# Performance work log

Hardware: AMD Instinct MI355X
Metric: run time of the kernel (lower is better)

## Reference

```python
import jax, jax.numpy as jnp
import numpy as np

BITS = 4
GROUP_SIZE = 128
INFEATURES = 4096
OUTFEATURES = 11008
ELEMS_PER_INT = 32 // BITS  # 8


def setup_inputs() -> dict:
    key = jax.random.key(0)
    k1, k2, k3, k4, k5 = jax.random.split(key, 5)
    x = jax.random.normal(k1, (4, 2048, INFEATURES), dtype=jnp.float32)
    # packed uint32 weights stored as int32 bit-pattern (full 32-bit random)
    qweight = jax.random.randint(k2, (OUTFEATURES, INFEATURES * BITS // 32), 0, 2147483647, dtype=jnp.int32)
    scales = jax.random.uniform(k3, (OUTFEATURES, INFEATURES // GROUP_SIZE), dtype=jnp.float32).astype(jnp.float16)
    biases = (jax.random.normal(k4, (OUTFEATURES, INFEATURES // GROUP_SIZE), dtype=jnp.float32) * 0.1).astype(jnp.float16)
    lin_bias = (jax.random.normal(k5, (OUTFEATURES,), dtype=jnp.float32) * 0.02).astype(jnp.float16)
    return {"x": x, "qweight": qweight, "scales": scales, "biases": biases, "lin_bias": lin_bias}


def _unpack(qweight):
    """Unpack [O, packed] int32 words -> [O, INFEATURES] int codes in [0, 2^BITS)."""
    w_u = jax.lax.bitcast_convert_type(qweight, jnp.uint32)  # logical bit view
    shifts = (jnp.arange(ELEMS_PER_INT, dtype=jnp.uint32) * BITS)  # [8]
    mask = jnp.uint32((1 << BITS) - 1)
    unpacked = (w_u[:, :, None] >> shifts) & mask  # [O, packed, 8]
    return unpacked.reshape(qweight.shape[0], -1)[:, :INFEATURES]


def reference(x, qweight, scales, biases, lin_bias):
    O = qweight.shape[0]
    G = scales.shape[1]
    q = _unpack(qweight).astype(jnp.float32)  # [O, INFEATURES]
    # group-wise dequant: w = scale * q + bias (per group of GROUP_SIZE input channels)
    qg = q.reshape(O, G, GROUP_SIZE)
    w = scales.astype(jnp.float32)[:, :, None] * qg + biases.astype(jnp.float32)[:, :, None]
    w = w.reshape(O, INFEATURES)
    out = jnp.einsum('bsi,oi->bso', x, w) + lin_bias.astype(jnp.float32)
    return out
```

## Files before the change

kernel.cpp:

```cpp
#include <hip/hip_runtime.h>
#include <hip/hip_fp16.h>
#include <stdint.h>

#define K_DIM 4096
#define N_DIM 11008
#define WPR   512
#define NGRP  32

typedef _Float16 half8 __attribute__((ext_vector_type(8)));
typedef float floatx4 __attribute__((ext_vector_type(4)));
typedef int   intx4  __attribute__((ext_vector_type(4)));
typedef int   intx16 __attribute__((ext_vector_type(16)));
union H8 { __half2 h2[4]; half8 v; };

#define GLOAD16(g, l) __builtin_amdgcn_global_load_lds( \
    (const __attribute__((address_space(1))) uint32_t*)(g), \
    (__attribute__((address_space(3))) uint32_t*)(l), 16, 0, 0)


static __device__ __forceinline__ uint32_t pack4(int a, int b, int c, int d) {
    return (uint32_t)(a & 255) | ((uint32_t)(b & 255) << 8) |
           ((uint32_t)(c & 255) << 16) | ((uint32_t)(d & 255) << 24);
}

__global__ __launch_bounds__(256)
void cvt_xq(const float* __restrict__ x, int8_t* __restrict__ xq,
            float* __restrict__ sx) {
    const int wid = threadIdx.x >> 6, lane = threadIdx.x & 63;
    const int row = blockIdx.x * 4 + wid;
    const float4* xr = (const float4*)(x + (size_t)row * K_DIM + lane * 64);
    float v[64];
    float amax = 0.f;
    #pragma unroll
    for (int i = 0; i < 16; ++i) {
        float4 f = xr[i];
        v[4*i] = f.x; v[4*i+1] = f.y; v[4*i+2] = f.z; v[4*i+3] = f.w;
        amax = fmaxf(amax, fmaxf(fmaxf(fabsf(f.x), fabsf(f.y)),
                                 fmaxf(fabsf(f.z), fabsf(f.w))));
    }
    #pragma unroll
    for (int m = 32; m; m >>= 1) amax = fmaxf(amax, __shfl_xor(amax, m));
    amax = fmaxf(amax, 1e-20f);
    const float inv = 127.0f / amax;
    uint32_t d[16];
    #pragma unroll
    for (int j = 0; j < 16; ++j)
        d[j] = pack4((int)rintf(v[4*j] * inv),   (int)rintf(v[4*j+1] * inv),
                     (int)rintf(v[4*j+2] * inv), (int)rintf(v[4*j+3] * inv));
    uint4* dst = (uint4*)xq;
    #pragma unroll
    for (int c2 = 0; c2 < 2; ++c2)
        #pragma unroll
        for (int h = 0; h < 2; ++h) {
            const size_t u = (size_t)(row >> 5) * 8192 +
                             (size_t)((lane * 2 + c2) * 64 + h * 32 + (row & 31));
            const int j0 = (c2 * 2 + h) * 4;
            dst[u] = make_uint4(d[j0], d[j0+1], d[j0+2], d[j0+3]);
        }
    if (lane == 0) sx[row] = amax * (1.0f / 127.0f);
}

__global__ __launch_bounds__(256)
void deq_wq(const uint32_t* __restrict__ qw, const float* __restrict__ scales,
            const float* __restrict__ biases, int8_t* __restrict__ wq,
            float* __restrict__ sw) {
    const int wid = threadIdx.x >> 6, lane = threadIdx.x & 63;
    const int row = blockIdx.x * 4 + wid;
    const uint4* qr = (const uint4*)(qw + (size_t)row * WPR) + lane * 2;
    const uint4 q0 = qr[0], q1 = qr[1];
    const int g = lane >> 1;
    const float s  = scales[(size_t)row * NGRP + g];
    const float bb = biases[(size_t)row * NGRP + g];
    const uint32_t uw[8] = {q0.x, q0.y, q0.z, q0.w, q1.x, q1.y, q1.z, q1.w};
    float v[64];
    float amax = 0.f;
    #pragma unroll
    for (int w8 = 0; w8 < 8; ++w8) {
        const uint32_t u = uw[w8];
        #pragma unroll
        for (int e = 0; e < 8; ++e) {
            const float val = fmaf(s, (float)((u >> (4 * e)) & 15u), bb);
            v[w8 * 8 + e] = val;
            amax = fmaxf(amax, fabsf(val));
        }
    }
    #pragma unroll
    for (int m = 32; m; m >>= 1) amax = fmaxf(amax, __shfl_xor(amax, m));
    amax = fmaxf(amax, 1e-20f);
    const float inv = 127.0f / amax;
    uint32_t d[16];
    #pragma unroll
    for (int j = 0; j < 16; ++j)
        d[j] = pack4((int)rintf(v[4*j] * inv),   (int)rintf(v[4*j+1] * inv),
                     (int)rintf(v[4*j+2] * inv), (int)rintf(v[4*j+3] * inv));
    uint4* dst = (uint4*)wq;
    #pragma unroll
    for (int c2 = 0; c2 < 2; ++c2)
        #pragma unroll
        for (int h = 0; h < 2; ++h) {
            const size_t u = (size_t)(row >> 5) * 8192 +
                             (size_t)((lane * 2 + c2) * 64 + h * 32 + (row & 31));
            const int j0 = (c2 * 2 + h) * 4;
            dst[u] = make_uint4(d[j0], d[j0+1], d[j0+2], d[j0+3]);
        }
    if (lane == 0) sw[row] = amax * (1.0f / 127.0f);
}

__global__ __launch_bounds__(512, 2)
void qlin17(const int8_t* __restrict__ xq, const int8_t* __restrict__ wq,
            const float* __restrict__ sx, const float* __restrict__ sw,
            const float* __restrict__ linb, float* __restrict__ out)
{
    __shared__ int8_t LD[2][65536];

    const int nwg = gridDim.x;
    int b = blockIdx.x;
    if ((nwg & 7) == 0) b = (b & 7) * (nwg >> 3) + (b >> 3);
    const int NBN = N_DIM / 256;
    const int bn = b % NBN;
    const int bm = b / NBN;

    const int tid  = threadIdx.x;
    const int lane = tid & 63;
    const int wid  = tid >> 6;
    const int wr   = wid >> 2;
    const int wc   = wid & 3;

    const int8_t* aG = xq + ((size_t)(bm * 8 + (tid >> 8)) * 8192
                             + (size_t)(((tid >> 6) & 3) * 64 + (tid & 63))) * 16;
    const int8_t* bG = wq + ((size_t)(bn * 8 + (tid >> 8)) * 8192
                             + (size_t)(((tid >> 6) & 3) * 64 + (tid & 63))) * 16;

    intx16 acc[4][2] = {};

    auto STG_A = [&](int kt, int h) {
        const int k = (kt < 32) ? kt : 0;
        const int8_t* g = aG + (size_t)h * 524288 + (size_t)k * 4096;
        int8_t* l = &LD[kt & 1][(h * 1024 + tid) * 16];
        GLOAD16(g, l);
        GLOAD16(g + 262144, l + 8192);
    };
    auto STG_B = [&](int kt, int h) {
        const int k = (kt < 32) ? kt : 0;
        const int8_t* g = bG + (size_t)h * 524288 + (size_t)k * 4096;
        int8_t* l = &LD[kt & 1][32768 + (h * 1024 + tid) * 16];
        GLOAD16(g, l);
        GLOAD16(g + 262144, l + 8192);
    };

    auto RDA = [&](intx4 (&A)[2][4], int buf, int mh) {
        const int8_t* Lb = &LD[buf][0];
        #pragma unroll
        for (int mf = 0; mf < 2; ++mf)
            #pragma unroll
            for (int ks = 0; ks < 4; ++ks)
                A[mf][ks] = *(const intx4*)(Lb +
                    (size_t)(((wr * 4 + mh * 2 + mf) * 256 + ks * 64 + lane) * 16));
    };
    auto RDB = [&](intx4 (&B)[4], int buf, int nh) {
        const int8_t* Lb = &LD[buf][32768];
        #pragma unroll
        for (int ks = 0; ks < 4; ++ks)
            B[ks] = *(const intx4*)(Lb +
                (size_t)(((wc * 2 + nh) * 256 + ks * 64 + lane) * 16));
    };
    auto MMQ = [&](const intx4 (&A)[2][4], const intx4 (&B)[4], int mh, int nh) {
        __builtin_amdgcn_s_setprio(1);
        #pragma unroll
        for (int ks = 0; ks < 4; ++ks)
            #pragma unroll
            for (int mf = 0; mf < 2; ++mf)
                acc[mh * 2 + mf][nh] = __builtin_amdgcn_mfma_i32_32x32x32_i8(
                    A[mf][ks], B[ks], acc[mh * 2 + mf][nh], 0, 0, 0);
        __builtin_amdgcn_s_setprio(0);
        __builtin_amdgcn_sched_barrier(0);
    };

    #define BAR()  __builtin_amdgcn_s_barrier()
    #define LGKM0() do { asm volatile("s_waitcnt lgkmcnt(0)" ::: "memory"); \
                         __builtin_amdgcn_sched_barrier(0); } while (0)

    STG_A(0, 0); STG_A(0, 1); STG_B(0, 0); STG_B(0, 1);
    STG_B(1, 0); STG_B(1, 1);
    asm volatile("s_waitcnt vmcnt(4)" ::: "memory");
    BAR();

    intx4 Aa[2][4], Ab[2][4], Ba[4], Bb[4];

    for (int t = 0; t < 32; ++t) {
        const int buf = t & 1;
        RDA(Aa, buf, 0); RDB(Ba, buf, 0); STG_A(t + 1, 0);
        asm volatile("s_waitcnt lgkmcnt(8)" ::: "memory");
        BAR(); LGKM0(); MMQ(Aa, Ba, 0, 0); BAR();
        RDB(Bb, buf, 1); STG_A(t + 1, 1);
        BAR(); LGKM0(); MMQ(Aa, Bb, 0, 1); BAR();
        RDA(Ab, buf, 1); STG_B(t + 2, 0);
        BAR(); LGKM0(); MMQ(Ab, Bb, 1, 1); BAR();
        STG_B(t + 2, 1);
        BAR(); LGKM0(); MMQ(Ab, Ba, 1, 0);
        asm volatile("s_waitcnt vmcnt(4)" ::: "memory");
        BAR();
    }
    asm volatile("s_waitcnt vmcnt(0)" ::: "memory");

    const int colb = bn * 256 + wc * 64 + (lane & 31);
    const int rowb = bm * 256 + wr * 128 + 4 * (lane >> 5);
    float swc[2], lbc[2];
    #pragma unroll
    for (int nf = 0; nf < 2; ++nf) {
        swc[nf] = sw[colb + nf * 32];
        lbc[nf] = linb[colb + nf * 32];
    }
    #pragma unroll
    for (int mf = 0; mf < 4; ++mf) {
        #pragma unroll
        for (int reg = 0; reg < 16; ++reg) {
            const int row = rowb + mf * 32 + (reg & 3) + 8 * (reg >> 2);
            const float sxr = sx[row];
            #pragma unroll
            for (int nf = 0; nf < 2; ++nf) {
                const int col = colb + nf * 32;
                out[(size_t)row * N_DIM + col] =
                    (float)acc[mf][nf][reg] * (sxr * swc[nf]) + lbc[nf];
            }
        }
    }
    #undef BAR
    #undef LGKM0
}

#define BM 128
#define BN 128
#define BK 64
#define NKT (K_DIM / BK)

__global__ __launch_bounds__(256)
void cvt_x(const float* __restrict__ x, _Float16* __restrict__ xh) {
    size_t i = (size_t)blockIdx.x * blockDim.x + threadIdx.x;
    const float4* p = (const float4*)(x + i * 8);
    float4 a = p[0], b = p[1];
    H8 h;
    h.h2[0] = __floats2half2_rn(a.x, b.x);
    h.h2[1] = __floats2half2_rn(a.y, b.y);
    h.h2[2] = __floats2half2_rn(a.z, b.z);
    h.h2[3] = __floats2half2_rn(a.w, b.w);
    *(half8*)(xh + i * 8) = h.v;
}

__global__ __launch_bounds__(256, 2)
void qlin_f16(const _Float16* __restrict__ xh,
              const uint32_t* __restrict__ qw,
              const float* __restrict__ scales,
              const float* __restrict__ biases,
              const float* __restrict__ linb,
              float* __restrict__ out)
{
    __shared__ _Float16 Asf[2][BM * BK];
    __shared__ _Float16 Bsf[2][BN * BK];

    const int NBN = N_DIM / BN;
    const int bn = blockIdx.x % NBN;
    const int bm = blockIdx.x / NBN;
    const int tid  = threadIdx.x;
    const int lane = tid & 63;
    const int wv   = tid >> 6;
    const int wm   = (wv >> 1) * 64;
    const int wn   = (wv & 1) * 64;

    const int arow = wv * 32 + (lane >> 3);
    const int acs  = ((lane & 7) ^ ((lane >> 3) & 7)) * 8;
    const _Float16* aSrc = xh + (size_t)(bm * BM + arow) * K_DIM + acs;

    const int srow = tid >> 1;
    const int bsel = tid & 1;
    const uint32_t* qB = qw + (size_t)(bn * BN + srow) * WPR + bsel * 4;
    const float*    sB = scales + (size_t)(bn * BN + srow) * NGRP;
    const float*    bB = biases + (size_t)(bn * BN + srow) * NGRP;
    const int bwbase = srow * BK;
    const int bswz   = srow & 7;

    floatx4 acc[4][4] = {};
    uint4 q0, q1; float s0, b0, s1, b1;

    auto LOADB = [&](uint4& qr, float& s, float& bb, int kt) {
        qr = *(const uint4*)(qB + kt * 8);
        s = sB[kt >> 1]; bb = bB[kt >> 1];
    };
    auto GLOADA = [&](int buf, int kt) {
        const _Float16* sp = aSrc + (size_t)kt * BK;
        #pragma unroll
        for (int j = 0; j < 4; ++j)
            GLOAD16(sp + (size_t)j * 8 * K_DIM, &Asf[buf][wv * 2048 + j * 512]);
    };
    auto DEQ = [&](const uint4& qr, float sf, float bf, int buf) {
        const __half2 s2 = __half2half2(__float2half(sf));
        const __half2 b2 = __half2half2(__float2half(bf));
        const __half2 c1024 = __float2half2_rn(1024.0f);
        const uint32_t uws[4] = {qr.x, qr.y, qr.z, qr.w};
        #pragma unroll
        for (int wi = 0; wi < 4; ++wi) {
            const uint32_t u = uws[wi];
            H8 h;
            #pragma unroll
            for (int p = 0; p < 4; ++p) {
                const uint32_t v = ((u >> (4 * p)) & 0x000F000Fu) | 0x64006400u;
                const __half2 q2 = __hsub2(__builtin_bit_cast(__half2, v), c1024);
                h.h2[p] = __hfma2(s2, q2, b2);
            }
            const int c = bsel * 4 + wi;
            *(half8*)&Bsf[buf][bwbase + ((c ^ bswz) * 8)] = h.v;
        }
    };
    const int fr = lane & 15;
    const int kq = lane >> 4;
    auto COMPUTE = [&](int buf) {
        const _Float16* Ab = &Asf[buf][0];
        const _Float16* Bb = &Bsf[buf][0];
        #pragma unroll
        for (int ks = 0; ks < 2; ++ks) {
            half8 af[4], bf[4];
            const int csx = ks * 4 + kq;
            #pragma unroll
            for (int i = 0; i < 4; ++i) {
                const int r = wm + i * 16 + fr;
                af[i] = *(const half8*)(Ab + r * BK + ((csx ^ (r & 7)) * 8));
            }
            #pragma unroll
            for (int i = 0; i < 4; ++i) {
                const int r = wn + i * 16 + fr;
                bf[i] = *(const half8*)(Bb + r * BK + ((csx ^ (r & 7)) * 8));
            }
            #pragma unroll
            for (int mf = 0; mf < 4; ++mf)
                #pragma unroll
                for (int nf = 0; nf < 4; ++nf)
                    acc[mf][nf] = __builtin_amdgcn_mfma_f32_16x16x32_f16(
                        af[mf], bf[nf], acc[mf][nf], 0, 0, 0);
        }
    };

    LOADB(q0, s0, b0, 0);
    GLOADA(0, 0);
    DEQ(q0, s0, b0, 0);
    LOADB(q0, s0, b0, 1);
    __syncthreads();
    for (int kt = 0; kt < NKT; kt += 2) {
        GLOADA(1, kt + 1);
        if (kt + 2 < NKT) LOADB(q1, s1, b1, kt + 2);
        DEQ(q0, s0, b0, 1);
        COMPUTE(0);
        __syncthreads();
        if (kt + 2 < NKT) {
            GLOADA(0, kt + 2);
            if (kt + 3 < NKT) LOADB(q0, s0, b0, kt + 3);
            DEQ(q1, s1, b1, 0);
        }
        COMPUTE(1);
        if (kt + 2 < NKT) __syncthreads();
    }
    const int rb = bm * BM + wm + ((lane >> 4) << 2);
    const int cb = bn * BN + wn + (lane & 15);
    #pragma unroll
    for (int nf = 0; nf < 4; ++nf) {
        const int col = cb + nf * 16;
        const float lb = linb[col];
        #pragma unroll
        for (int mf = 0; mf < 4; ++mf) {
            const int row = rb + mf * 16;
            #pragma unroll
            for (int j = 0; j < 4; ++j)
                out[(size_t)(row + j) * N_DIM + col] = acc[mf][nf][j] + lb;
        }
    }
}

extern "C" void kernel_launch(void* const* d_in, const int* in_sizes, int n_in,
                              void* d_out, int out_size, void* d_ws, size_t ws_size,
                              hipStream_t stream) {
    const float*    x      = (const float*)d_in[0];
    const uint32_t* qw     = (const uint32_t*)d_in[1];
    const float*    scales = (const float*)d_in[2];
    const float*    biases = (const float*)d_in[3];
    const float*    linb   = (const float*)d_in[4];
    float*          out    = (float*)d_out;

    const int M = in_sizes[0] / K_DIM;
    const size_t XB = (size_t)M * K_DIM;
    const size_t WB = (size_t)N_DIM * K_DIM;
    const size_t needQ = XB + WB + (size_t)(M + N_DIM) * 4;
    const size_t needF = (size_t)M * K_DIM * sizeof(_Float16);

    if (ws_size >= needQ && (M % 256) == 0) {
        int8_t* xqp = (int8_t*)d_ws;
        int8_t* wqp = xqp + XB;
        float*  sxp = (float*)(xqp + XB + WB);
        float*  swp = sxp + M;
        cvt_xq<<<M / 4, 256, 0, stream>>>(x, xqp, sxp);
        deq_wq<<<N_DIM / 4, 256, 0, stream>>>(qw, scales, biases, wqp, swp);
        dim3 grid((M / 256) * (N_DIM / 256));
        qlin17<<<grid, 512, 0, stream>>>(xqp, wqp, sxp, swp, linb, out);
    } else if (ws_size >= needF && (M % BM) == 0) {
        _Float16* xh = (_Float16*)d_ws;
        cvt_x<<<(unsigned)((size_t)M * K_DIM / 8 / 256), 256, 0, stream>>>(x, xh);
        dim3 grid((M / BM) * (N_DIM / BN));
        qlin_f16<<<grid, 256, 0, stream>>>(xh, qw, scales, biases, linb, out);
    }
}
```

Measured before the change: 463.2 us.

## Shrink int8 GEMM tile to 128x128 with smaller LDS for higher occupancy

```diff
diff --git a/kernel.cpp b/kernel.cpp
--- a/kernel.cpp
+++ b/kernel.cpp
@@ -106,17 +106,17 @@
     if (lane == 0) sw[row] = amax * (1.0f / 127.0f);
 }
 
-__global__ __launch_bounds__(512, 2)
-void qlin17(const int8_t* __restrict__ xq, const int8_t* __restrict__ wq,
+__global__ __launch_bounds__(512, 4)
+void qlin19(const int8_t* __restrict__ xq, const int8_t* __restrict__ wq,
             const float* __restrict__ sx, const float* __restrict__ sw,
             const float* __restrict__ linb, float* __restrict__ out)
 {
-    __shared__ int8_t LD[2][65536];
+    __shared__ int8_t LD[2][32768];
 
     const int nwg = gridDim.x;
     int b = blockIdx.x;
     if ((nwg & 7) == 0) b = (b & 7) * (nwg >> 3) + (b >> 3);
-    const int NBN = N_DIM / 256;
+    const int NBN = N_DIM / 128;
     const int bn = b % NBN;
     const int bm = b / NBN;
 
@@ -126,52 +126,46 @@
     const int wr   = wid >> 2;
     const int wc   = wid & 3;
 
-    const int8_t* aG = xq + ((size_t)(bm * 8 + (tid >> 8)) * 8192
-                             + (size_t)(((tid >> 6) & 3) * 64 + (tid & 63))) * 16;
-    const int8_t* bG = wq + ((size_t)(bn * 8 + (tid >> 8)) * 8192
-                             + (size_t)(((tid >> 6) & 3) * 64 + (tid & 63))) * 16;
-
-    intx16 acc[4][2] = {};
-
-    auto STG_A = [&](int kt, int h) {
+    const int8_t* aS = xq + ((size_t)(bm * 4 + (tid >> 8)) * 8192 + (size_t)(tid & 255)) * 16;
+    const int8_t* bS = wq + ((size_t)(bn * 4 + (tid >> 8)) * 8192 + (size_t)(tid & 255)) * 16;
+
+    intx16 acc[2] = {};
+
+    auto STG_A = [&](int kt) {
         const int k = (kt < 32) ? kt : 0;
-        const int8_t* g = aG + (size_t)h * 524288 + (size_t)k * 4096;
-        int8_t* l = &LD[kt & 1][(h * 1024 + tid) * 16];
+        const int8_t* g = aS + (size_t)k * 4096;
+        int8_t* l = &LD[kt & 1][tid * 16];
         GLOAD16(g, l);
         GLOAD16(g + 262144, l + 8192);
     };
-    auto STG_B = [&](int kt, int h) {
+    auto STG_B = [&](int kt) {
         const int k = (kt < 32) ? kt : 0;
-        const int8_t* g = bG + (size_t)h * 524288 + (size_t)k * 4096;
-        int8_t* l = &LD[kt & 1][32768 + (h * 1024 + tid) * 16];
+        const int8_t* g = bS + (size_t)k * 4096;
+        int8_t* l = &LD[kt & 1][16384 + tid * 16];
         GLOAD16(g, l);
         GLOAD16(g + 262144, l + 8192);
     };
 
-    auto RDA = [&](intx4 (&A)[2][4], int buf, int mh) {
+    auto RDA = [&](intx4 (&A)[4], int buf, int mf) {
         const int8_t* Lb = &LD[buf][0];
         #pragma unroll
-        for (int mf = 0; mf < 2; ++mf)
-            #pragma unroll
-            for (int ks = 0; ks < 4; ++ks)
-                A[mf][ks] = *(const intx4*)(Lb +
-                    (size_t)(((wr * 4 + mh * 2 + mf) * 256 + ks * 64 + lane) * 16));
-    };
-    auto RDB = [&](intx4 (&B)[4], int buf, int nh) {
-        const int8_t* Lb = &LD[buf][32768];
+        for (int ks = 0; ks < 4; ++ks)
+            A[ks] = *(const intx4*)(Lb +
+                (size_t)((((wr * 2 + mf) * 4 + ks) * 64 + lane) * 16));
+    };
+    auto RDB = [&](intx4 (&B)[4], int buf) {
+        const int8_t* Lb = &LD[buf][16384];
         #pragma unroll
         for (int ks = 0; ks < 4; ++ks)
             B[ks] = *(const intx4*)(Lb +
-                (size_t)(((wc * 2 + nh) * 256 + ks * 64 + lane) * 16));
-    };
-    auto MMQ = [&](const intx4 (&A)[2][4], const intx4 (&B)[4], int mh, int nh) {
+                (size_t)(((wc * 4 + ks) * 64 + lane) * 16));
+    };
+    auto MMQ = [&](const intx4 (&A)[4], const intx4 (&B)[4], int mf) {
         __builtin_amdgcn_s_setprio(1);
         #pragma unroll
         for (int ks = 0; ks < 4; ++ks)
-            #pragma unroll
-            for (int mf = 0; mf < 2; ++mf)
-                acc[mh * 2 + mf][nh] = __builtin_amdgcn_mfma_i32_32x32x32_i8(
-                    A[mf][ks], B[ks], acc[mh * 2 + mf][nh], 0, 0, 0);
+            acc[mf] = __builtin_amdgcn_mfma_i32_32x32x32_i8(
+                A[ks], B[ks], acc[mf], 0, 0, 0);
         __builtin_amdgcn_s_setprio(0);
         __builtin_amdgcn_sched_barrier(0);
     };
@@ -180,49 +174,33 @@
     #define LGKM0() do { asm volatile("s_waitcnt lgkmcnt(0)" ::: "memory"); \
                          __builtin_amdgcn_sched_barrier(0); } while (0)
 
-    STG_A(0, 0); STG_A(0, 1); STG_B(0, 0); STG_B(0, 1);
-    STG_B(1, 0); STG_B(1, 1);
-    asm volatile("s_waitcnt vmcnt(4)" ::: "memory");
+    STG_A(0); STG_B(0);
+    asm volatile("s_waitcnt vmcnt(0)" ::: "memory");
     BAR();
 
-    intx4 Aa[2][4], Ab[2][4], Ba[4], Bb[4];
+    intx4 A0[4], A1[4], Bq[4];
 
     for (int t = 0; t < 32; ++t) {
         const int buf = t & 1;
-        RDA(Aa, buf, 0); RDB(Ba, buf, 0); STG_A(t + 1, 0);
-        asm volatile("s_waitcnt lgkmcnt(8)" ::: "memory");
-        BAR(); LGKM0(); MMQ(Aa, Ba, 0, 0); BAR();
-        RDB(Bb, buf, 1); STG_A(t + 1, 1);
-        BAR(); LGKM0(); MMQ(Aa, Bb, 0, 1); BAR();
-        RDA(Ab, buf, 1); STG_B(t + 2, 0);
-        BAR(); LGKM0(); MMQ(Ab, Bb, 1, 1); BAR();
-        STG_B(t + 2, 1);
-        BAR(); LGKM0(); MMQ(Ab, Ba, 1, 0);
-        asm volatile("s_waitcnt vmcnt(4)" ::: "memory");
+        RDA(A0, buf, 0); RDB(Bq, buf); STG_A(t + 1);
+        BAR(); LGKM0(); MMQ(A0, Bq, 0); BAR();
+        RDA(A1, buf, 1); STG_B(t + 1);
+        BAR(); LGKM0(); MMQ(A1, Bq, 1);
+        asm volatile("s_waitcnt vmcnt(0)" ::: "memory");
         BAR();
     }
-    asm volatile("s_waitcnt vmcnt(0)" ::: "memory");
-
-    const int colb = bn * 256 + wc * 64 + (lane & 31);
-    const int rowb = bm * 256 + wr * 128 + 4 * (lane >> 5);
-    float swc[2], lbc[2];
-    #pragma unroll
-    for (int nf = 0; nf < 2; ++nf) {
-        swc[nf] = sw[colb + nf * 32];
-        lbc[nf] = linb[colb + nf * 32];
-    }
-    #pragma unroll
-    for (int mf = 0; mf < 4; ++mf) {
+
+    const int col  = bn * 128 + wc * 32 + (lane & 31);
+    const int rowb = bm * 128 + wr * 64 + 4 * (lane >> 5);
+    const float swc = sw[col];
+    const float lbc = linb[col];
+    #pragma unroll
+    for (int mf = 0; mf < 2; ++mf) {
         #pragma unroll
         for (int reg = 0; reg < 16; ++reg) {
             const int row = rowb + mf * 32 + (reg & 3) + 8 * (reg >> 2);
-            const float sxr = sx[row];
-            #pragma unroll
-            for (int nf = 0; nf < 2; ++nf) {
-                const int col = colb + nf * 32;
-                out[(size_t)row * N_DIM + col] =
-                    (float)acc[mf][nf][reg] * (sxr * swc[nf]) + lbc[nf];
-            }
+            out[(size_t)row * N_DIM + col] =
+                (float)acc[mf][reg] * (sx[row] * swc) + lbc;
         }
     }
     #undef BAR
@@ -397,8 +375,8 @@
         float*  swp = sxp + M;
         cvt_xq<<<M / 4, 256, 0, stream>>>(x, xqp, sxp);
         deq_wq<<<N_DIM / 4, 256, 0, stream>>>(qw, scales, biases, wqp, swp);
-        dim3 grid((M / 256) * (N_DIM / 256));
-        qlin17<<<grid, 512, 0, stream>>>(xqp, wqp, sxp, swp, linb, out);
+        dim3 grid((M / 128) * (N_DIM / 128));
+        qlin19<<<grid, 512, 0, stream>>>(xqp, wqp, sxp, swp, linb, out);
     } else if (ws_size >= needF && (M % BM) == 0) {
         _Float16* xh = (_Float16*)d_ws;
         cvt_x<<<(unsigned)((size_t)M * K_DIM / 8 / 256), 256, 0, stream>>>(x, xh);
```

Result: slower. 564.6 us (+21.9%).

## Shrink int8 GEMM tile to 256x128 with 4 waves and triple-buffered LDS

Applied to the files above, without the earlier changes.

```diff
diff --git a/kernel.cpp b/kernel.cpp
--- a/kernel.cpp
+++ b/kernel.cpp
@@ -106,72 +106,76 @@
     if (lane == 0) sw[row] = amax * (1.0f / 127.0f);
 }
 
-__global__ __launch_bounds__(512, 2)
-void qlin17(const int8_t* __restrict__ xq, const int8_t* __restrict__ wq,
+__global__ __launch_bounds__(256, 2)
+void qlin21(const int8_t* __restrict__ xq, const int8_t* __restrict__ wq,
             const float* __restrict__ sx, const float* __restrict__ sw,
             const float* __restrict__ linb, float* __restrict__ out)
 {
-    __shared__ int8_t LD[2][65536];
+    __shared__ int8_t LD[3][24576];
 
     const int nwg = gridDim.x;
     int b = blockIdx.x;
     if ((nwg & 7) == 0) b = (b & 7) * (nwg >> 3) + (b >> 3);
-    const int NBN = N_DIM / 256;
+    const int NBN = N_DIM / 128;
     const int bn = b % NBN;
     const int bm = b / NBN;
 
     const int tid  = threadIdx.x;
     const int lane = tid & 63;
     const int wid  = tid >> 6;
-    const int wr   = wid >> 2;
-    const int wc   = wid & 3;
-
-    const int8_t* aG = xq + ((size_t)(bm * 8 + (tid >> 8)) * 8192
-                             + (size_t)(((tid >> 6) & 3) * 64 + (tid & 63))) * 16;
-    const int8_t* bG = wq + ((size_t)(bn * 8 + (tid >> 8)) * 8192
-                             + (size_t)(((tid >> 6) & 3) * 64 + (tid & 63))) * 16;
+    const int wr   = wid >> 1;
+    const int wc   = wid & 1;
+
+    const int8_t* aG = xq + ((size_t)(bm * 8 + (tid >> 7)) * 8192 + (size_t)(tid & 127)) * 16;
+    const int8_t* bG = wq + ((size_t)(bn * 4 + (tid >> 7)) * 8192 + (size_t)(tid & 127)) * 16;
 
     intx16 acc[4][2] = {};
 
-    auto STG_A = [&](int kt, int h) {
-        const int k = (kt < 32) ? kt : 0;
-        const int8_t* g = aG + (size_t)h * 524288 + (size_t)k * 4096;
-        int8_t* l = &LD[kt & 1][(h * 1024 + tid) * 16];
-        GLOAD16(g, l);
-        GLOAD16(g + 262144, l + 8192);
-    };
-    auto STG_B = [&](int kt, int h) {
-        const int k = (kt < 32) ? kt : 0;
-        const int8_t* g = bG + (size_t)h * 524288 + (size_t)k * 4096;
-        int8_t* l = &LD[kt & 1][32768 + (h * 1024 + tid) * 16];
-        GLOAD16(g, l);
-        GLOAD16(g + 262144, l + 8192);
-    };
-
-    auto RDA = [&](intx4 (&A)[2][4], int buf, int mh) {
+    auto STG_A = [&](int t) {
+        const int kt = (t < 64) ? t : 0;
+        const int8_t* g = aG + (size_t)kt * 2048;
+        int8_t* l = &LD[t % 3][tid * 16];
+        #pragma unroll
+        for (int j = 0; j < 4; ++j)
+            GLOAD16(g + (size_t)j * 2 * 8192 * 16, l + j * 4096);
+    };
+    auto STG_B = [&](int t) {
+        const int kt = (t < 64) ? t : 0;
+        const int8_t* g = bG + (size_t)kt * 2048;
+        int8_t* l = &LD[t % 3][16384 + tid * 16];
+        #pragma unroll
+        for (int j = 0; j < 2; ++j)
+            GLOAD16(g + (size_t)j * 2 * 8192 * 16, l + j * 4096);
+    };
+
+    auto RDA = [&](intx4 (&A)[2][2], int buf, int mh) {
         const int8_t* Lb = &LD[buf][0];
         #pragma unroll
         for (int mf = 0; mf < 2; ++mf)
             #pragma unroll
-            for (int ks = 0; ks < 4; ++ks)
+            for (int ks = 0; ks < 2; ++ks)
                 A[mf][ks] = *(const intx4*)(Lb +
-                    (size_t)(((wr * 4 + mh * 2 + mf) * 256 + ks * 64 + lane) * 16));
-    };
-    auto RDB = [&](intx4 (&B)[4], int buf, int nh) {
-        const int8_t* Lb = &LD[buf][32768];
-        #pragma unroll
-        for (int ks = 0; ks < 4; ++ks)
-            B[ks] = *(const intx4*)(Lb +
-                (size_t)(((wc * 2 + nh) * 256 + ks * 64 + lane) * 16));
-    };
-    auto MMQ = [&](const intx4 (&A)[2][4], const intx4 (&B)[4], int mh, int nh) {
+                    (size_t)(((wr * 4 + mh * 2 + mf) * 128 + ks * 64 + lane) * 16));
+    };
+    auto RDB = [&](intx4 (&B)[2][2], int buf) {
+        const int8_t* Lb = &LD[buf][16384];
+        #pragma unroll
+        for (int nf = 0; nf < 2; ++nf)
+            #pragma unroll
+            for (int ks = 0; ks < 2; ++ks)
+                B[nf][ks] = *(const intx4*)(Lb +
+                    (size_t)(((wc * 2 + nf) * 128 + ks * 64 + lane) * 16));
+    };
+    auto MMQ = [&](const intx4 (&A)[2][2], const intx4 (&B)[2][2], int mh) {
         __builtin_amdgcn_s_setprio(1);
         #pragma unroll
-        for (int ks = 0; ks < 4; ++ks)
+        for (int ks = 0; ks < 2; ++ks)
             #pragma unroll
             for (int mf = 0; mf < 2; ++mf)
-                acc[mh * 2 + mf][nh] = __builtin_amdgcn_mfma_i32_32x32x32_i8(
-                    A[mf][ks], B[ks], acc[mh * 2 + mf][nh], 0, 0, 0);
+                #pragma unroll
+                for (int nf = 0; nf < 2; ++nf)
+                    acc[mh * 2 + mf][nf] = __builtin_amdgcn_mfma_i32_32x32x32_i8(
+                        A[mf][ks], B[nf][ks], acc[mh * 2 + mf][nf], 0, 0, 0);
         __builtin_amdgcn_s_setprio(0);
         __builtin_amdgcn_sched_barrier(0);
     };
@@ -180,30 +184,25 @@
     #define LGKM0() do { asm volatile("s_waitcnt lgkmcnt(0)" ::: "memory"); \
                          __builtin_amdgcn_sched_barrier(0); } while (0)
 
-    STG_A(0, 0); STG_A(0, 1); STG_B(0, 0); STG_B(0, 1);
-    STG_B(1, 0); STG_B(1, 1);
-    asm volatile("s_waitcnt vmcnt(4)" ::: "memory");
+    STG_A(0); STG_B(0);
+    STG_A(1); STG_B(1);
+    asm volatile("s_waitcnt vmcnt(6)" ::: "memory");
     BAR();
 
-    intx4 Aa[2][4], Ab[2][4], Ba[4], Bb[4];
-
-    for (int t = 0; t < 32; ++t) {
-        const int buf = t & 1;
-        RDA(Aa, buf, 0); RDB(Ba, buf, 0); STG_A(t + 1, 0);
-        asm volatile("s_waitcnt lgkmcnt(8)" ::: "memory");
-        BAR(); LGKM0(); MMQ(Aa, Ba, 0, 0); BAR();
-        RDB(Bb, buf, 1); STG_A(t + 1, 1);
-        BAR(); LGKM0(); MMQ(Aa, Bb, 0, 1); BAR();
-        RDA(Ab, buf, 1); STG_B(t + 2, 0);
-        BAR(); LGKM0(); MMQ(Ab, Bb, 1, 1); BAR();
-        STG_B(t + 2, 1);
-        BAR(); LGKM0(); MMQ(Ab, Ba, 1, 0);
-        asm volatile("s_waitcnt vmcnt(4)" ::: "memory");
+    intx4 Aa[2][2], Ab[2][2], Bq[2][2];
+
+    for (int t = 0; t < 64; ++t) {
+        const int buf = t % 3;
+        RDA(Aa, buf, 0); RDB(Bq, buf); STG_A(t + 2);
+        BAR(); LGKM0(); MMQ(Aa, Bq, 0); BAR();
+        RDA(Ab, buf, 1); STG_B(t + 2);
+        BAR(); LGKM0(); MMQ(Ab, Bq, 1);
+        asm volatile("s_waitcnt vmcnt(6)" ::: "memory");
         BAR();
     }
     asm volatile("s_waitcnt vmcnt(0)" ::: "memory");
 
-    const int colb = bn * 256 + wc * 64 + (lane & 31);
+    const int colb = bn * 128 + wc * 64 + (lane & 31);
     const int rowb = bm * 256 + wr * 128 + 4 * (lane >> 5);
     float swc[2], lbc[2];
     #pragma unroll
@@ -397,8 +396,8 @@
         float*  swp = sxp + M;
         cvt_xq<<<M / 4, 256, 0, stream>>>(x, xqp, sxp);
         deq_wq<<<N_DIM / 4, 256, 0, stream>>>(qw, scales, biases, wqp, swp);
-        dim3 grid((M / 256) * (N_DIM / 256));
-        qlin17<<<grid, 512, 0, stream>>>(xqp, wqp, sxp, swp, linb, out);
+        dim3 grid((M / 256) * (N_DIM / 128));
+        qlin21<<<grid, 256, 0, stream>>>(xqp, wqp, sxp, swp, linb, out);
     } else if (ws_size >= needF && (M % BM) == 0) {
         _Float16* xh = (_Float16*)d_ws;
         cvt_x<<<(unsigned)((size_t)M * K_DIM / 8 / 256), 256, 0, stream>>>(x, xh);
```

Result: faster. 453.1 us (median of 2 runs) (-2.2%).
